# Kernel optimization log

Hardware: AMD Instinct MI355X
Metric: run time of the kernel (lower is better)

Reference implementation:

```python
import jax, jax.numpy as jnp
import numpy as np

B, C, H, W = 8, 512, 64, 64
KD, VD, OD = 64, 512, 512
BN_EPS = 1e-5


def setup_inputs() -> dict:
    key = jax.random.key(0)
    ks = jax.random.split(key, 10)
    s = lambda fan_in: 1.0 / np.sqrt(fan_in)
    return {
        "x": jax.random.normal(ks[0], (B, C, H, W), jnp.float32),
        "Wq": jax.random.normal(ks[1], (KD, C), jnp.float32) * s(C),
        "bq": jnp.zeros((KD,), jnp.float32),
        "Wk": jax.random.normal(ks[2], (KD, C), jnp.float32) * s(C),
        "bk": jnp.zeros((KD,), jnp.float32),
        "Wv": jax.random.normal(ks[3], (VD, C), jnp.float32) * s(C),
        "bv": jnp.zeros((VD,), jnp.float32),
        "gamma": jnp.zeros((1,), jnp.float32),  # torch init: zeros(1)
        "Wf": jax.random.normal(ks[4], (OD, VD), jnp.float32) * s(VD),
        "bn_w": jnp.ones((OD,), jnp.float32),
        "bn_b": jnp.zeros((OD,), jnp.float32),
        "bn_mean": jnp.zeros((OD,), jnp.float32),
        "bn_var": jnp.ones((OD,), jnp.float32),
    }


def reference(x, Wq, bq, Wk, bk, Wv, bv, gamma, Wf, bn_w, bn_b, bn_mean, bn_var):
    b, c, h, w = x.shape
    n = h * w
    # 1x1 convs == per-pixel channel matmuls
    q = jnp.einsum('bchw,kc->bkhw', x, Wq) + bq[None, :, None, None]  # [B,KD,H,W]
    k = jnp.einsum('bchw,kc->bkhw', x, Wk) + bk[None, :, None, None]
    v = jnp.einsum('bchw,vc->bvhw', x, Wv) + bv[None, :, None, None]
    q = q.reshape(b, -1, n)  # [B,KD,N]
    k = k.reshape(b, -1, n)
    v = v.reshape(b, -1, n)  # [B,VD,N]
    # energy[b, i, j] = q[:, :, i] . k[:, :, j]   (proj_query permuted)
    energy = jnp.einsum('bki,bkj->bij', q, k)  # [B,N,N]
    attention = jax.nn.softmax(energy, axis=-1)
    # out = value @ attention^T : out[b, v, i] = sum_j value[b, v, j] * attention[b, i, j]
    out = jnp.einsum('bvj,bij->bvi', v, attention)  # [B,VD,N]
    out = out.reshape(b, c, h, w)
    out = gamma * out + x
    # fuse: 1x1 conv (no bias) -> BatchNorm (inference) -> ReLU
    fused = jnp.einsum('bchw,oc->bohw', out, Wf)
    inv = jax.lax.rsqrt(bn_var + BN_EPS)
    fused = (fused - bn_mean[None, :, None, None]) * (bn_w * inv)[None, :, None, None] + bn_b[None, :, None, None]
    return jax.nn.relu(fused)
```

## Files before the change

### kernel.cpp

```cpp
#include <hip/hip_runtime.h>
#include <hip/hip_bf16.h>

typedef unsigned short u16;
typedef unsigned int u32;
typedef __attribute__((ext_vector_type(8))) short bf16x8;
typedef __attribute__((ext_vector_type(4))) float f32x4;
typedef __attribute__((ext_vector_type(4))) u16 u16x4;

#define B_ 8
#define C_ 512
#define N_ 4096
#define KD_ 64
#define VD_ 512
#define OD_ 512

static __device__ __forceinline__ float bf2f(u16 u) {
    union { u32 i; float f; } z; z.i = ((u32)u) << 16; return z.f;
}
static __device__ __forceinline__ u16 f2bf(float f) {
    union { float f; u32 u; } v; v.f = f;
    u32 r = v.u + 0x7fffu + ((v.u >> 16) & 1u);
    return (u16)(r >> 16);
}
static __device__ __forceinline__ u32 pkbf(float lo, float hi) {
    u32 ul = __float_as_uint(lo) + 0x8000u;
    u32 uh = __float_as_uint(hi) + 0x8000u;
    return __builtin_amdgcn_perm(uh, ul, 0x07060302u);
}
static __device__ __forceinline__ int swz(int row) { return ((row >> 2) + (row >> 4)) & 3; }

__global__ __launch_bounds__(256) void transpose_convert_kernel(
    const float* __restrict__ x, const float* __restrict__ Wf,
    const float* __restrict__ gamma,
    u16* __restrict__ xT, u16* __restrict__ Wf16)
{
    const int bid = blockIdx.x;
    if (bid >= 4096) {
        const int tid = (bid - 4096) * 256 + threadIdx.x;
        const float4* src = (const float4*)Wf + (size_t)tid * 16;
        u16* dst = Wf16 + (size_t)tid * 64;
        #pragma unroll
        for (int j = 0; j < 16; j++) {
            const float4 f = src[j];
            u16x4 p;
            p[0] = f2bf(f.x); p[1] = f2bf(f.y); p[2] = f2bf(f.z); p[3] = f2bf(f.w);
            *(u16x4*)(dst + j * 4) = p;
        }
        return;
    }
    if (gamma[0] == 0.0f) return;
    __shared__ u32 tile[64][33];
    const int nt = bid & 63;
    const int ct = (bid >> 6) & 7;
    const int b  = bid >> 9;
    const float* xb  = x  + ((size_t)b * C_ + ct * 64) * N_ + nt * 64;
    u16*         xTb = xT + ((size_t)b * N_ + nt * 64) * C_ + ct * 64;
    const int t = threadIdx.x;
    {
        const int p  = t >> 3;
        const int n8 = t & 7;
        const float* r0 = xb + (size_t)(2 * p)     * N_ + n8 * 8;
        const float* r1 = xb + (size_t)(2 * p + 1) * N_ + n8 * 8;
        const float4 a0 = *(const float4*)(r0);
        const float4 a1 = *(const float4*)(r0 + 4);
        const float4 c0 = *(const float4*)(r1);
        const float4 c1 = *(const float4*)(r1 + 4);
        const float av[8] = { a0.x, a0.y, a0.z, a0.w, a1.x, a1.y, a1.z, a1.w };
        const float cv[8] = { c0.x, c0.y, c0.z, c0.w, c1.x, c1.y, c1.z, c1.w };
        #pragma unroll
        for (int j = 0; j < 8; j++)
            tile[n8 * 8 + j][p] = (u32)f2bf(av[j]) | ((u32)f2bf(cv[j]) << 16);
    }
    __syncthreads();
    #pragma unroll
    for (int h = 0; h < 2; h++) {
        const int id = t + h * 256;
        const int n  = id >> 3;
        const int q  = id & 7;
        uint4 val;
        val.x = tile[n][q * 4 + 0];
        val.y = tile[n][q * 4 + 1];
        val.z = tile[n][q * 4 + 2];
        val.w = tile[n][q * 4 + 3];
        *(uint4*)(xTb + (size_t)n * C_ + q * 8) = val;
    }
}

__global__ __launch_bounds__(256) void proj_kernel(
    const u16* __restrict__ xT,
    const float* __restrict__ Wq, const float* __restrict__ bq,
    const float* __restrict__ Wk, const float* __restrict__ bk,
    const float* __restrict__ Wv, const float* __restrict__ bv,
    const float* __restrict__ gamma,
    u16* __restrict__ q, u16* __restrict__ k, u16* __restrict__ v)
{
    if (gamma[0] == 0.0f) return;
    const int b = blockIdx.x >> 6;
    const int p = (blockIdx.x & 63) * 64 + (threadIdx.x & 63);
    const int dg = threadIdx.x >> 6;
    const u16* xrow = xT + ((size_t)b * N_ + p) * C_;
    for (int d0 = dg * 160; d0 < dg * 160 + 160; d0++) {
        const float* wrow; float bias; u16* dst; int dd; int dim;
        if (d0 < 64)       { dd = d0;       wrow = Wq + (size_t)dd * C_; bias = bq[dd]; dst = q; dim = KD_; }
        else if (d0 < 128) { dd = d0 - 64;  wrow = Wk + (size_t)dd * C_; bias = bk[dd]; dst = k; dim = KD_; }
        else               { dd = d0 - 128; wrow = Wv + (size_t)dd * C_; bias = bv[dd]; dst = v; dim = VD_; }
        float s = bias;
        for (int c = 0; c < C_; c++) s += bf2f(xrow[c]) * wrow[c];
        dst[((size_t)b * dim + dd) * N_ + p] = f2bf(s);
    }
}

__global__ __launch_bounds__(256) void attn_kernel(
    const u16* __restrict__ xT, const u16* __restrict__ q,
    const u16* __restrict__ k, const u16* __restrict__ v,
    const float* __restrict__ gamma, u16* __restrict__ yT)
{
    const float g = gamma[0];
    if (g == 0.0f) return;
    __shared__ float pls[4][64];
    const int wv = threadIdx.x >> 6, lane = threadIdx.x & 63;
    const int b  = blockIdx.x >> 7;
    const int q0 = (blockIdx.x & 127) * 32 + wv * 8;
    const u16* kb = k + (size_t)b * KD_ * N_;
    const u16* vb = v + (size_t)b * VD_ * N_;
    for (int qi = 0; qi < 8; qi++) {
        const int i = q0 + qi;
        const float qv = bf2f(q[((size_t)b * KD_ + lane) * N_ + i]);
        float mx = -1e30f, l = 0.f;
        for (int jb = 0; jb < N_; jb += 64) {
            float e = 0.f;
            for (int kd = 0; kd < 64; kd++)
                e += __shfl(qv, kd) * bf2f(kb[(size_t)kd * N_ + jb + lane]);
            const float nm = fmaxf(mx, e);
            l = l * __expf(mx - nm) + __expf(e - nm);
            mx = nm;
        }
        for (int off = 32; off; off >>= 1) {
            const float mo = __shfl_xor(mx, off);
            const float lo = __shfl_xor(l, off);
            const float nm = fmaxf(mx, mo);
            l = l * __expf(mx - nm) + lo * __expf(mo - nm);
            mx = nm;
        }
        float oacc[8];
        #pragma unroll
        for (int r = 0; r < 8; r++) oacc[r] = 0.f;
        for (int jb = 0; jb < N_; jb += 64) {
            float e = 0.f;
            for (int kd = 0; kd < 64; kd++)
                e += __shfl(qv, kd) * bf2f(kb[(size_t)kd * N_ + jb + lane]);
            __syncthreads();
            pls[wv][lane] = __expf(e - mx);
            __syncthreads();
            for (int jj = 0; jj < 64; jj++) {
                const float p = pls[wv][jj];
                #pragma unroll
                for (int r = 0; r < 8; r++)
                    oacc[r] += p * bf2f(vb[(size_t)(r * 64 + lane) * N_ + jb + jj]);
            }
        }
        const float inv = 1.f / l;
        #pragma unroll
        for (int r = 0; r < 8; r++) {
            const size_t idx = ((size_t)b * N_ + i) * C_ + r * 64 + lane;
            yT[idx] = f2bf(g * oacc[r] * inv + bf2f(xT[idx]));
        }
    }
}

__global__ __launch_bounds__(256, 3) void gemm_bn_relu(
    const float* __restrict__ x, const u16* __restrict__ yT,
    const u16* __restrict__ Wf16, const float* __restrict__ gamma,
    const float* __restrict__ bnw, const float* __restrict__ bnb,
    const float* __restrict__ bnm, const float* __restrict__ bnv,
    float* __restrict__ out)
{
    __shared__ u16 lds_x[128 * 32];
    __shared__ u16 lds_w[128 * 32];

    const int bid = blockIdx.x;
    const int pt8 = bid & 7;
    const int ot  = (bid >> 3) & 3;
    const int g   = bid >> 5;
    const int pt  = (g & 3) * 8 + pt8;
    const int b   = g >> 2;

    const int t = threadIdx.x;
    const int lane = t & 63;
    const int wv = t >> 6;
    const int wm = wv >> 1;
    const int wn = wv & 1;
    const int lcol = lane & 15;
    const int kq = lane >> 4;

    const int rw = t >> 2, posw = t & 3;
    const int ql = (posw - swz(rw)) & 3;
    const u16* WT0 = Wf16 + (size_t)(ot * 128 + rw) * C_ + ql * 8;
    const u16* WT1 = WT0 + (size_t)64 * C_;
    const int wla0 = rw * 32 + posw * 8;
    const int wla1 = wla0 + 64 * 32;

    int aaddr[4], baddr[4];
    #pragma unroll
    for (int i = 0; i < 4; i++) {
        const int P = wm * 64 + i * 16 + lcol;
        aaddr[i] = P * 32 + ((kq + swz(P)) & 3) * 8;
        const int R = wn * 64 + i * 16 + lcol;
        baddr[i] = R * 32 + ((kq + swz(R)) & 3) * 8;
    }

    f32x4 acc[4][4];
    #pragma unroll
    for (int i = 0; i < 4; i++)
        #pragma unroll
        for (int j = 0; j < 4; j++)
            acc[i][j] = (f32x4){0.f, 0.f, 0.f, 0.f};

    auto compute = [&]() {
        bf16x8 af[4], bfg[4];
        #pragma unroll
        for (int mi = 0; mi < 4; mi++)
            af[mi] = *(const bf16x8*)&lds_x[aaddr[mi]];
        #pragma unroll
        for (int ni = 0; ni < 4; ni++)
            bfg[ni] = *(const bf16x8*)&lds_w[baddr[ni]];
        #pragma unroll
        for (int mi = 0; mi < 4; mi++)
            #pragma unroll
            for (int ni = 0; ni < 4; ni++)
                acc[mi][ni] = __builtin_amdgcn_mfma_f32_16x16x32_bf16(
                    af[mi], bfg[ni], acc[mi][ni], 0, 0, 0);
    };

    if (gamma[0] == 0.0f) {
        const int q4 = t & 15, cp = t >> 4;
        u32* lx32 = (u32*)lds_x;
        int xidx[8];
        #pragma unroll
        for (int j = 0; j < 8; j++) {
            const int p = q4 + 16 * j;
            xidx[j] = p * 16 + (((cp >> 2) + swz(p)) & 3) * 4 + (cp & 3);
        }
        const float* eA = x + ((size_t)b * C_ + 2 * cp) * N_ + pt * 128 + q4;
        const float* oA = eA + N_;
        const float* eB = eA + (size_t)32 * N_;
        const float* oB = oA + (size_t)32 * N_;

        float evA[8], odA[8], evB[8], odB[8];
        #pragma unroll
        for (int j = 0; j < 8; j++) { evA[j] = eA[16 * j]; odA[j] = oA[16 * j]; }
        #pragma unroll
        for (int j = 0; j < 8; j++) { evB[j] = eB[16 * j]; odB[j] = oB[16 * j]; }
        eA += (size_t)64 * N_; oA += (size_t)64 * N_;
        eB += (size_t)64 * N_; oB += (size_t)64 * N_;
        uint4 w0 = *(const uint4*)(WT0);
        uint4 w1 = *(const uint4*)(WT1);

        for (int ks = 0; ks < 16; ks += 2) {
            __syncthreads();
            #pragma unroll
            for (int j = 0; j < 8; j++) lx32[xidx[j]] = pkbf(evA[j], odA[j]);
            *(uint4*)&lds_w[wla0] = w0;
            *(uint4*)&lds_w[wla1] = w1;
            if (ks + 2 < 16) {
                #pragma unroll
                for (int j = 0; j < 8; j++) { evA[j] = eA[16 * j]; odA[j] = oA[16 * j]; }
                eA += (size_t)64 * N_; oA += (size_t)64 * N_;
            }
            w0 = *(const uint4*)(WT0 + (ks + 1) * 32);
            w1 = *(const uint4*)(WT1 + (ks + 1) * 32);
            __syncthreads();
            compute();
            __syncthreads();
            #pragma unroll
            for (int j = 0; j < 8; j++) lx32[xidx[j]] = pkbf(evB[j], odB[j]);
            *(uint4*)&lds_w[wla0] = w0;
            *(uint4*)&lds_w[wla1] = w1;
            if (ks + 3 < 16) {
                #pragma unroll
                for (int j = 0; j < 8; j++) { evB[j] = eB[16 * j]; odB[j] = oB[16 * j]; }
                eB += (size_t)64 * N_; oB += (size_t)64 * N_;
            }
            if (ks + 2 < 16) {
                w0 = *(const uint4*)(WT0 + (ks + 2) * 32);
                w1 = *(const uint4*)(WT1 + (ks + 2) * 32);
            }
            __syncthreads();
            compute();
        }
    } else {
        const u16* YT0 = yT + ((size_t)b * N_ + pt * 128 + rw) * C_ + ql * 8;
        const u16* YT1 = YT0 + (size_t)64 * C_;
        uint4 x0 = *(const uint4*)YT0, x1 = *(const uint4*)YT1;
        uint4 w0 = *(const uint4*)WT0, w1 = *(const uint4*)WT1;
        for (int ks = 0; ks < 16; ks++) {
            __syncthreads();
            *(uint4*)&lds_x[wla0] = x0;
            *(uint4*)&lds_x[wla1] = x1;
            *(uint4*)&lds_w[wla0] = w0;
            *(uint4*)&lds_w[wla1] = w1;
            if (ks + 1 < 16) {
                x0 = *(const uint4*)(YT0 + (ks + 1) * 32);
                x1 = *(const uint4*)(YT1 + (ks + 1) * 32);
                w0 = *(const uint4*)(WT0 + (ks + 1) * 32);
                w1 = *(const uint4*)(WT1 + (ks + 1) * 32);
            }
            __syncthreads();
            compute();
        }
    }

    float scale[4], shift[4];
    #pragma unroll
    for (int ni = 0; ni < 4; ni++) {
        const int o = ot * 128 + wn * 64 + ni * 16 + lcol;
        const float s = bnw[o] * rsqrtf(bnv[o] + 1e-5f);
        scale[ni] = s;
        shift[ni] = bnb[o] - bnm[o] * s;
    }
    #pragma unroll
    for (int mi = 0; mi < 4; mi++) {
        const int npix = pt * 128 + wm * 64 + mi * 16 + kq * 4;
        #pragma unroll
        for (int ni = 0; ni < 4; ni++) {
            const int o = ot * 128 + wn * 64 + ni * 16 + lcol;
            f32x4 pk;
            #pragma unroll
            for (int r = 0; r < 4; r++)
                pk[r] = fmaxf(acc[mi][ni][r] * scale[ni] + shift[ni], 0.0f);
            *(f32x4*)(out + ((size_t)b * OD_ + o) * N_ + npix) = pk;
        }
    }
}

extern "C" void kernel_launch(void* const* d_in, const int* in_sizes, int n_in,
                              void* d_out, int out_size, void* d_ws, size_t ws_size,
                              hipStream_t stream) {
    const float* x     = (const float*)d_in[0];
    const float* Wq    = (const float*)d_in[1];
    const float* bq    = (const float*)d_in[2];
    const float* Wk    = (const float*)d_in[3];
    const float* bk    = (const float*)d_in[4];
    const float* Wv    = (const float*)d_in[5];
    const float* bv    = (const float*)d_in[6];
    const float* gamma = (const float*)d_in[7];
    const float* Wf    = (const float*)d_in[8];
    const float* bnw   = (const float*)d_in[9];
    const float* bnb   = (const float*)d_in[10];
    const float* bnm   = (const float*)d_in[11];
    const float* bnv   = (const float*)d_in[12];
    float* out = (float*)d_out;

    char* ws = (char*)d_ws;
    u16* xT   = (u16*)(ws);
    u16* Wf16 = (u16*)(ws + 33554432);
    u16* yT   = (u16*)(ws + 34078720);
    u16* q    = (u16*)(ws + 67633152);
    u16* k    = (u16*)(ws + 71827456);
    u16* v    = (u16*)(ws + 76021760);

    transpose_convert_kernel<<<4112, 256, 0, stream>>>(x, Wf, gamma, xT, Wf16);
    proj_kernel<<<512, 256, 0, stream>>>(xT, Wq, bq, Wk, bk, Wv, bv, gamma, q, k, v);
    attn_kernel<<<1024, 256, 0, stream>>>(xT, q, k, v, gamma, yT);
    gemm_bn_relu<<<1024, 256, 0, stream>>>(x, yT, Wf16, gamma, bnw, bnb, bnm, bnv, out);
}
```

Before: 164.8 us.

## Double-buffer LDS in gamma==0 GEMM path with one barrier per k-step

Splits the LDS staging buffers into two halves so the gamma==0 path of the fused conv+BN+ReLU GEMM writes the next k-slice into one buffer while MFMAs read the other. This drops from two barriers to one per k-step, and the barrier is an explicit lgkmcnt wait plus s_barrier. Occupancy hint is raised from 3 to 4 blocks per SM. The doubled LDS footprint and the register pressure from the larger launch bound may limit gains or cause spills.

```diff
diff --git a/kernel.cpp b/kernel.cpp
--- a/kernel.cpp
+++ b/kernel.cpp
@@ -13,6 +13,8 @@
 #define KD_ 64
 #define VD_ 512
 #define OD_ 512
+
+#define SYNC_LDS() asm volatile("s_waitcnt lgkmcnt(0)\ns_barrier" ::: "memory")
 
 static __device__ __forceinline__ float bf2f(u16 u) {
     union { u32 i; float f; } z; z.i = ((u32)u) << 16; return z.f;
@@ -168,15 +170,15 @@
     }
 }
 
-__global__ __launch_bounds__(256, 3) void gemm_bn_relu(
+__global__ __launch_bounds__(256, 4) void gemm_bn_relu(
     const float* __restrict__ x, const u16* __restrict__ yT,
     const u16* __restrict__ Wf16, const float* __restrict__ gamma,
     const float* __restrict__ bnw, const float* __restrict__ bnb,
     const float* __restrict__ bnm, const float* __restrict__ bnv,
     float* __restrict__ out)
 {
-    __shared__ u16 lds_x[128 * 32];
-    __shared__ u16 lds_w[128 * 32];
+    __shared__ u16 lds_x[2][128 * 32];
+    __shared__ u16 lds_w[2][128 * 32];
 
     const int bid = blockIdx.x;
     const int pt8 = bid & 7;
@@ -216,14 +218,14 @@
         for (int j = 0; j < 4; j++)
             acc[i][j] = (f32x4){0.f, 0.f, 0.f, 0.f};
 
-    auto compute = [&]() {
+    auto compute = [&](const u16* bx, const u16* bw) {
         bf16x8 af[4], bfg[4];
         #pragma unroll
         for (int mi = 0; mi < 4; mi++)
-            af[mi] = *(const bf16x8*)&lds_x[aaddr[mi]];
+            af[mi] = *(const bf16x8*)&bx[aaddr[mi]];
         #pragma unroll
         for (int ni = 0; ni < 4; ni++)
-            bfg[ni] = *(const bf16x8*)&lds_w[baddr[ni]];
+            bfg[ni] = *(const bf16x8*)&bw[baddr[ni]];
         #pragma unroll
         for (int mi = 0; mi < 4; mi++)
             #pragma unroll
@@ -234,59 +236,69 @@
 
     if (gamma[0] == 0.0f) {
         const int q4 = t & 15, cp = t >> 4;
-        u32* lx32 = (u32*)lds_x;
         int xidx[8];
         #pragma unroll
         for (int j = 0; j < 8; j++) {
             const int p = q4 + 16 * j;
             xidx[j] = p * 16 + (((cp >> 2) + swz(p)) & 3) * 4 + (cp & 3);
         }
-        const float* eA = x + ((size_t)b * C_ + 2 * cp) * N_ + pt * 128 + q4;
-        const float* oA = eA + N_;
-        const float* eB = eA + (size_t)32 * N_;
-        const float* oB = oA + (size_t)32 * N_;
-
-        float evA[8], odA[8], evB[8], odB[8];
-        #pragma unroll
-        for (int j = 0; j < 8; j++) { evA[j] = eA[16 * j]; odA[j] = oA[16 * j]; }
-        #pragma unroll
-        for (int j = 0; j < 8; j++) { evB[j] = eB[16 * j]; odB[j] = oB[16 * j]; }
-        eA += (size_t)64 * N_; oA += (size_t)64 * N_;
-        eB += (size_t)64 * N_; oB += (size_t)64 * N_;
-        uint4 w0 = *(const uint4*)(WT0);
-        uint4 w1 = *(const uint4*)(WT1);
-
-        for (int ks = 0; ks < 16; ks += 2) {
-            __syncthreads();
+        const float* pb = x + ((size_t)(b * C_ + 2 * cp)) * N_ + pt * 128 + q4;
+        const size_t kstep = (size_t)32 * N_;
+
+        float ev[2][8], od[2][8];
+        uint4 wr[2][2];
+        #pragma unroll
+        for (int j = 0; j < 8; j++) { ev[0][j] = pb[16 * j];         od[0][j] = pb[N_ + 16 * j]; }
+        #pragma unroll
+        for (int j = 0; j < 8; j++) { ev[1][j] = pb[kstep + 16 * j]; od[1][j] = pb[kstep + N_ + 16 * j]; }
+        wr[0][0] = *(const uint4*)(WT0);      wr[0][1] = *(const uint4*)(WT1);
+        wr[1][0] = *(const uint4*)(WT0 + 32); wr[1][1] = *(const uint4*)(WT1 + 32);
+
+        {
+            u32* lx = (u32*)lds_x[0];
             #pragma unroll
-            for (int j = 0; j < 8; j++) lx32[xidx[j]] = pkbf(evA[j], odA[j]);
-            *(uint4*)&lds_w[wla0] = w0;
-            *(uint4*)&lds_w[wla1] = w1;
-            if (ks + 2 < 16) {
+            for (int j = 0; j < 8; j++) lx[xidx[j]] = pkbf(ev[0][j], od[0][j]);
+            *(uint4*)&lds_w[0][wla0] = wr[0][0];
+            *(uint4*)&lds_w[0][wla1] = wr[0][1];
+        }
+        #pragma unroll
+        for (int j = 0; j < 8; j++) { ev[0][j] = pb[2 * kstep + 16 * j]; od[0][j] = pb[2 * kstep + N_ + 16 * j]; }
+        wr[0][0] = *(const uint4*)(WT0 + 64); wr[0][1] = *(const uint4*)(WT1 + 64);
+        SYNC_LDS();
+
+        for (int it = 0; it < 8; it++) {
+            compute(lds_x[0], lds_w[0]);
+            {
+                u32* lx = (u32*)lds_x[1];
                 #pragma unroll
-                for (int j = 0; j < 8; j++) { evA[j] = eA[16 * j]; odA[j] = oA[16 * j]; }
-                eA += (size_t)64 * N_; oA += (size_t)64 * N_;
-            }
-            w0 = *(const uint4*)(WT0 + (ks + 1) * 32);
-            w1 = *(const uint4*)(WT1 + (ks + 1) * 32);
-            __syncthreads();
-            compute();
-            __syncthreads();
-            #pragma unroll
-            for (int j = 0; j < 8; j++) lx32[xidx[j]] = pkbf(evB[j], odB[j]);
-            *(uint4*)&lds_w[wla0] = w0;
-            *(uint4*)&lds_w[wla1] = w1;
-            if (ks + 3 < 16) {
+                for (int j = 0; j < 8; j++) lx[xidx[j]] = pkbf(ev[1][j], od[1][j]);
+                *(uint4*)&lds_w[1][wla0] = wr[1][0];
+                *(uint4*)&lds_w[1][wla1] = wr[1][1];
+            }
+            if (it < 7) {
+                const size_t o = (size_t)(2 * it + 3) * kstep;
                 #pragma unroll
-                for (int j = 0; j < 8; j++) { evB[j] = eB[16 * j]; odB[j] = oB[16 * j]; }
-                eB += (size_t)64 * N_; oB += (size_t)64 * N_;
-            }
-            if (ks + 2 < 16) {
-                w0 = *(const uint4*)(WT0 + (ks + 2) * 32);
-                w1 = *(const uint4*)(WT1 + (ks + 2) * 32);
-            }
-            __syncthreads();
-            compute();
+                for (int j = 0; j < 8; j++) { ev[1][j] = pb[o + 16 * j]; od[1][j] = pb[o + N_ + 16 * j]; }
+                wr[1][0] = *(const uint4*)(WT0 + (2 * it + 3) * 32);
+                wr[1][1] = *(const uint4*)(WT1 + (2 * it + 3) * 32);
+            }
+            SYNC_LDS();
+            compute(lds_x[1], lds_w[1]);
+            if (it < 7) {
+                u32* lx = (u32*)lds_x[0];
+                #pragma unroll
+                for (int j = 0; j < 8; j++) lx[xidx[j]] = pkbf(ev[0][j], od[0][j]);
+                *(uint4*)&lds_w[0][wla0] = wr[0][0];
+                *(uint4*)&lds_w[0][wla1] = wr[0][1];
+                if (it < 6) {
+                    const size_t o = (size_t)(2 * it + 4) * kstep;
+                    #pragma unroll
+                    for (int j = 0; j < 8; j++) { ev[0][j] = pb[o + 16 * j]; od[0][j] = pb[o + N_ + 16 * j]; }
+                    wr[0][0] = *(const uint4*)(WT0 + (2 * it + 4) * 32);
+                    wr[0][1] = *(const uint4*)(WT1 + (2 * it + 4) * 32);
+                }
+                SYNC_LDS();
+            }
         }
     } else {
         const u16* YT0 = yT + ((size_t)b * N_ + pt * 128 + rw) * C_ + ql * 8;
@@ -295,10 +307,10 @@
         uint4 w0 = *(const uint4*)WT0, w1 = *(const uint4*)WT1;
         for (int ks = 0; ks < 16; ks++) {
             __syncthreads();
-            *(uint4*)&lds_x[wla0] = x0;
-            *(uint4*)&lds_x[wla1] = x1;
-            *(uint4*)&lds_w[wla0] = w0;
-            *(uint4*)&lds_w[wla1] = w1;
+            *(uint4*)&lds_x[0][wla0] = x0;
+            *(uint4*)&lds_x[0][wla1] = x1;
+            *(uint4*)&lds_w[0][wla0] = w0;
+            *(uint4*)&lds_w[0][wla1] = w1;
             if (ks + 1 < 16) {
                 x0 = *(const uint4*)(YT0 + (ks + 1) * 32);
                 x1 = *(const uint4*)(YT1 + (ks + 1) * 32);
@@ -306,7 +318,7 @@
                 w1 = *(const uint4*)(WT1 + (ks + 1) * 32);
             }
             __syncthreads();
-            compute();
+            compute(lds_x[0], lds_w[0]);
         }
     }
 
```

Measured after the change: 271.8 us. 1.65x slower.
